# Performance work log

Measured on AMD Instinct MI355X. Metric: run time of the kernel, lower is better.

## Reference

```python
import jax, jax.numpy as jnp
import numpy as np

EPS = 1e-5  # torch InstanceNorm2d default eps

def instance_norm(x):
    # per-sample, per-channel normalization over spatial dims (affine=False)
    m = jnp.mean(x, axis=(2, 3), keepdims=True)
    v = jnp.var(x, axis=(2, 3), keepdims=True)
    return (x - m) * jax.lax.rsqrt(v + EPS)

def conv2d(x, w, b, stride, pad):
    y = jax.lax.conv_general_dilated(
        x, w, (stride, stride), [(pad, pad), (pad, pad)],
        dimension_numbers=('NCHW', 'OIHW', 'NCHW'))
    return y + b[None, :, None, None]

def res_block(x, w1, b1, w2, b2):
    out = conv2d(jax.nn.relu(instance_norm(x)), w1, b1, 1, 1)
    out = conv2d(jax.nn.relu(instance_norm(out)), w2, b2, 1, 1)
    return out + x

def res_block_strided(x, w1, b1, w2, b2, ws, bs):
    out = conv2d(jax.nn.relu(instance_norm(x)), w1, b1, 2, 1)
    out = conv2d(jax.nn.relu(instance_norm(out)), w2, b2, 1, 1)
    return out + conv2d(x, ws, bs, 2, 0)  # 1x1 strided skip projection

def setup_inputs() -> dict:
    key = jax.random.key(0)
    ks = jax.random.split(key, 12)
    B, N, C, H, W = 64, 1, 3, 256, 256
    TEXT, EMB, F, HEADS = 256, 512, 32, 5
    FH, FW = H // 16, W // 16  # 16, 16
    def rn(k, shape, scale=0.05):
        return jax.random.normal(k, shape, dtype=jnp.float32) * scale
    z = lambda *s: jnp.zeros(s, jnp.float32)
    return {
        'x': jax.random.normal(ks[0], (B, N, C, H, W), jnp.float32),
        'text_vector': jax.random.normal(ks[1], (B, TEXT), jnp.float32),
        'conv1_w': rn(ks[2], (F, C, 7, 7)),
        'conv1_b': z(F),
        'rbs_w1': rn(ks[3], (3, F, F, 3, 3)),  # 3 strided resblocks
        'rbs_b1': z(3, F),
        'rbs_w2': rn(ks[4], (3, F, F, 3, 3)),
        'rbs_b2': z(3, F),
        'rbs_ws': rn(ks[5], (3, F, F, 1, 1)),
        'rbs_bs': z(3, F),
        'rb_w1': rn(ks[6], (2, F, F, 3, 3)),  # 2 plain resblocks
        'rb_b1': z(2, F),
        'rb_w2': rn(ks[7], (2, F, F, 3, 3)),
        'rb_b2': z(2, F),
        'attn_w': rn(ks[8], (HEADS, FH * FW, TEXT)),  # torch Linear [out,in] per head
        'attn_b': z(HEADS, FH * FW),
        'final_w': rn(ks[9], (EMB, FH * FW * HEADS)),
        'final_b': z(EMB),
    }

def reference(x, text_vector, conv1_w, conv1_b, rbs_w1, rbs_b1, rbs_w2, rbs_b2,
              rbs_ws, rbs_bs, rb_w1, rb_b1, rb_w2, rb_b2, attn_w, attn_b,
              final_w, final_b):
    B, N, C, H, W = x.shape
    feat = x.reshape(B, N * C, H, W)
    feat = instance_norm(feat)
    feat = conv2d(feat, conv1_w, conv1_b, 2, 3)
    # block1 = strided + plain; block2 = strided + plain; block3 = strided
    feat = res_block_strided(feat, rbs_w1[0], rbs_b1[0], rbs_w2[0], rbs_b2[0], rbs_ws[0], rbs_bs[0])
    feat = res_block(feat, rb_w1[0], rb_b1[0], rb_w2[0], rb_b2[0])
    feat = res_block_strided(feat, rbs_w1[1], rbs_b1[1], rbs_w2[1], rbs_b2[1], rbs_ws[1], rbs_bs[1])
    feat = res_block(feat, rb_w1[1], rb_b1[1], rb_w2[1], rb_b2[1])
    feat = res_block_strided(feat, rbs_w1[2], rbs_b1[2], rbs_w2[2], rbs_b2[2], rbs_ws[2], rbs_bs[2])
    # feat: [B, 32, FH, FW]
    HEADS = attn_w.shape[0]
    FH, FW = feat.shape[2], feat.shape[3]
    # sigmoid-gated spatial attention logits per head: [B, HEADS, FH, FW]
    a = jax.nn.sigmoid(jnp.einsum('bt,hot->bho', text_vector, attn_w) + attn_b[None])
    a = a.reshape(B, HEADS, FH, FW)
    # channel scores: spatial sum of gate * feature -> [B, HEADS, C]
    scores = jnp.einsum('bhij,bcij->bhc', a, feat)
    probs = jax.nn.softmax(scores, axis=-1)  # old F.softmax over channel dim
    # weighted channel sum -> per-head attention map [B, HEADS, FH, FW]
    amaps = jnp.einsum('bhc,bcij->bhij', probs, feat)
    out = amaps.reshape(B, -1) @ final_w.T + final_b
    return out
```

## Files before the change

### kernel.cpp

```cpp
#include <hip/hip_runtime.h>
#include <cstdint>
#include <cstddef>

#define INORM_EPS 1e-5f

typedef _Float16 f16;
typedef f16 f16x8 __attribute__((ext_vector_type(8)));
typedef f16 f16x4 __attribute__((ext_vector_type(4)));
typedef float f32x4 __attribute__((ext_vector_type(4)));

__global__ __launch_bounds__(256) void prep_stats(
    const float* __restrict__ rbs_w1, const float* __restrict__ rbs_w2,
    const float* __restrict__ rb_w1, const float* __restrict__ rb_w2,
    const float* __restrict__ rbs_ws, const float* __restrict__ conv1_w,
    const float* __restrict__ x, float2* __restrict__ SP,
    f16* __restrict__ wp3, f16* __restrict__ wp1, f16* __restrict__ wp7,
    float2* __restrict__ SPx8) {
  const int bx = blockIdx.x;
  if (bx >= 480) {
    const int g = bx - 480;
    const int map = g >> 3, chunk = g & 7;
    const float4* p = (const float4*)(x + (size_t)map * 65536 + (size_t)chunk * 8192);
    float s = 0.f, ss = 0.f;
    for (int i = threadIdx.x; i < 2048; i += 256) {
      float4 v = p[i];
      s += v.x + v.y + v.z + v.w;
      ss += v.x * v.x + v.y * v.y + v.z * v.z + v.w * v.w;
    }
    __shared__ float r0[256], r1[256];
    r0[threadIdx.x] = s;
    r1[threadIdx.x] = ss;
    __syncthreads();
    for (int off = 128; off > 0; off >>= 1) {
      if ((int)threadIdx.x < off) {
        r0[threadIdx.x] += r0[threadIdx.x + off];
        r1[threadIdx.x] += r1[threadIdx.x + off];
      }
      __syncthreads();
    }
    if (threadIdx.x == 0) SPx8[map * 8 + chunk] = make_float2(r0[0], r1[0]);
    return;
  }
  int i = bx * 256 + threadIdx.x;
  if (i < 20480) { SP[i] = make_float2(0.f, 0.f); return; }
  i -= 20480;
  if (i < 92160) {
    int mat = i / 9216, r = i % 9216;
    int p = r >> 10, f = (r >> 9) & 1, l = (r >> 3) & 63, j = r & 7;
    int co = f * 16 + (l & 15), ci = (l >> 4) * 8 + j;
    const float* src; int m;
    if (mat < 3) { src = rbs_w1; m = mat; }
    else if (mat < 6) { src = rbs_w2; m = mat - 3; }
    else if (mat < 8) { src = rb_w1; m = mat - 6; }
    else { src = rb_w2; m = mat - 8; }
    wp3[i] = (f16)src[m * 9216 + co * 288 + ci * 9 + p];
    return;
  }
  i -= 92160;
  if (i < 3072) {
    int mat = i / 1024, r = i % 1024;
    int f = r >> 9, l = (r >> 3) & 63, j = r & 7;
    wp1[i] = (f16)rbs_ws[mat * 1024 + (f * 16 + (l & 15)) * 32 + (l >> 4) * 8 + j];
    return;
  }
  i -= 3072;
  if (i >= 7168) return;
  int ky = i >> 10, f = (i >> 9) & 1, l = (i >> 3) & 63, j = i & 7;
  int k = (l >> 4) * 8 + j, kx = k >> 2, ci = k & 3;
  float v = 0.f;
  if (kx < 7 && ci < 3) v = conv1_w[(f * 16 + (l & 15)) * 147 + ci * 49 + ky * 7 + kx];
  wp7[i] = (f16)v;
}

template <int W, int SKIP, int RPB>
__global__ __launch_bounds__(256) void conv3r(
    const f16* __restrict__ Rin, const float2* __restrict__ SPin, float inv_hw,
    const f16* __restrict__ wp, const float* __restrict__ bias,
    const float* __restrict__ bias2, const f16* __restrict__ skip,
    const f16* __restrict__ wps, f16* __restrict__ Rout,
    float2* __restrict__ ostats) {
  constexpr int TPR = W / 16;
  constexpr int LEN = (RPB * TPR) / 4;
  const int t = threadIdx.x, w = t >> 6, l = t & 63;
  const int n = l & 15, q = l >> 4;
  const int b = blockIdx.z;
  const int tx = w % TPR;
  const int y0 = blockIdx.x * RPB + (w / TPR) * LEN;
  const int x = (tx << 4) + n;
  const f16* Rb = Rin + (size_t)b * W * W * 32;

  f16x8 sc, sh;
#pragma unroll
  for (int j = 0; j < 8; j++) {
    float2 s = SPin[b * 32 + q * 8 + j];
    float mean = s.x * inv_hw;
    float rstd = rsqrtf(s.y * inv_hw - mean * mean + INORM_EPS);
    sc[j] = (f16)rstd;
    sh[j] = (f16)(-mean * rstd);
  }

  f16x8 wf[18];
#pragma unroll
  for (int i = 0; i < 18; i++) wf[i] = *(const f16x8*)(wp + i * 512 + l * 8);
  f16x8 wsf0, wsf1;
  if (SKIP == 2) {
    wsf0 = *(const f16x8*)(wps + l * 8);
    wsf1 = *(const f16x8*)(wps + 512 + l * 8);
  }
  float b0 = bias[n], b1 = bias[16 + n];
  if (SKIP == 2) { b0 += bias2[n]; b1 += bias2[16 + n]; }

  f16* ro = Rout + (size_t)b * W * W * 32;
  const f16* sb = skip ? skip + (size_t)b * (SKIP == 2 ? 4 : 1) * W * W * 32 : nullptr;

  bool okc[3];
#pragma unroll
  for (int kx = 0; kx < 3; kx++) okc[kx] = (unsigned)(x + kx - 1) < (unsigned)W;

  auto rowload = [&](int gy, f16x8* dst) {
    int gyc = min(max(gy, 0), W - 1);
#pragma unroll
    for (int kx = 0; kx < 3; kx++) {
      int gxc = min(max(x + kx - 1, 0), W - 1);
      dst[kx] = *(const f16x8*)(Rb + ((size_t)gyc * W + gxc) * 32 + q * 8);
    }
  };
  auto rownorm = [&](int gy, const f16x8* src, f16x8* dst) {
    bool okr = (unsigned)gy < (unsigned)W;
#pragma unroll
    for (int kx = 0; kx < 3; kx++) {
      f16x8 v = src[kx] * sc + sh;
#pragma unroll
      for (int e = 0; e < 8; e++) v[e] = v[e] > (f16)0 ? v[e] : (f16)0;
      f16x8 z = {};
      dst[kx] = (okr && okc[kx]) ? v : z;
    }
  };

  float sm0 = 0.f, sq0 = 0.f, sm1 = 0.f, sq1 = 0.f;
  f16x8 win[9];
  f16x8 pf[3][3];
#pragma unroll
  for (int jj = 0; jj < 3; jj++) rowload(y0 + jj - 1, &win[jj * 3]);
  if (LEN > 1) rowload(y0 + 2, pf[0]);
  if (LEN > 2) rowload(y0 + 3, pf[1]);
#pragma unroll
  for (int jj = 0; jj < 3; jj++) rownorm(y0 + jj - 1, &win[jj * 3], &win[jj * 3]);

#pragma unroll
  for (int i = 0; i < LEN; i++) {
    int y = y0 + i;
    if (i + 3 < LEN) rowload(y0 + i + 4, pf[(i + 2) % 3]);
    f32x4 acc0 = {0.f, 0.f, 0.f, 0.f}, acc1 = {0.f, 0.f, 0.f, 0.f};
#pragma unroll
    for (int ky = 0; ky < 3; ky++) {
      int slot = (i + ky) % 3;
#pragma unroll
      for (int kx = 0; kx < 3; kx++) {
        f16x8 a = win[slot * 3 + kx];
        acc0 = __builtin_amdgcn_mfma_f32_16x16x32_f16(a, wf[2 * (ky * 3 + kx)], acc0, 0, 0, 0);
        acc1 = __builtin_amdgcn_mfma_f32_16x16x32_f16(a, wf[2 * (ky * 3 + kx) + 1], acc1, 0, 0, 0);
      }
    }
    if (SKIP == 2) {
      const int Ws = 2 * W;
      f16x8 as = *(const f16x8*)(sb + ((size_t)(2 * y) * Ws + 2 * x) * 32 + q * 8);
      acc0 = __builtin_amdgcn_mfma_f32_16x16x32_f16(as, wsf0, acc0, 0, 0, 0);
      acc1 = __builtin_amdgcn_mfma_f32_16x16x32_f16(as, wsf1, acc1, 0, 0, 0);
    }
#pragma unroll
    for (int r = 0; r < 4; r++) {
      size_t px = (size_t)y * W + (tx << 4) + q * 4 + r;
      float v0 = acc0[r] + b0;
      float v1 = acc1[r] + b1;
      if (SKIP == 1) {
        v0 += (float)sb[px * 32 + n];
        v1 += (float)sb[px * 32 + 16 + n];
      }
      ro[px * 32 + n] = (f16)v0;
      ro[px * 32 + 16 + n] = (f16)v1;
      sm0 += v0; sq0 += v0 * v0;
      sm1 += v1; sq1 += v1 * v1;
    }
    if (i + 1 < LEN) rownorm(y0 + i + 2, pf[i % 3], &win[(i % 3) * 3]);
  }
  if (ostats) {
    sm0 += __shfl_xor(sm0, 16); sm0 += __shfl_xor(sm0, 32);
    sq0 += __shfl_xor(sq0, 16); sq0 += __shfl_xor(sq0, 32);
    sm1 += __shfl_xor(sm1, 16); sm1 += __shfl_xor(sm1, 32);
    sq1 += __shfl_xor(sq1, 16); sq1 += __shfl_xor(sq1, 32);
    if (l < 16) {
      atomicAdd(&ostats[b * 32 + n].x, sm0);
      atomicAdd(&ostats[b * 32 + n].y, sq0);
      atomicAdd(&ostats[b * 32 + 16 + n].x, sm1);
      atomicAdd(&ostats[b * 32 + 16 + n].y, sq1);
    }
  }
}

template <int WIN, int STRIDE, int SKIP, int RPB>
__global__ __launch_bounds__(256) void conv3n(
    const f16* __restrict__ Rin, const float2* __restrict__ SPin, float inv_hw,
    const f16* __restrict__ wp, const float* __restrict__ bias,
    const float* __restrict__ bias2, const f16* __restrict__ skip,
    const f16* __restrict__ wps, f16* __restrict__ Rout,
    float2* __restrict__ ostats) {
  constexpr int WOUT = WIN / STRIDE;
  constexpr int TPR = WOUT / 16;
  constexpr int UNITS = TPR * RPB;
  constexpr int U = UNITS / 4;
  static_assert(U >= 1, "need at least one unit per wave");
  constexpr int NB = (U >= 3) ? 3 : ((U >= 2) ? 2 : 1);
  const int t = threadIdx.x, w = t >> 6, l = t & 63;
  const int n = l & 15, q = l >> 4;
  const int b = blockIdx.z;
  const int yb = blockIdx.x * RPB;
  const f16* Rb = Rin + (size_t)b * WIN * WIN * 32;

  f16x8 sc, sh;
#pragma unroll
  for (int j = 0; j < 8; j++) {
    float2 s = SPin[b * 32 + q * 8 + j];
    float mean = s.x * inv_hw;
    float rstd = rsqrtf(s.y * inv_hw - mean * mean + INORM_EPS);
    sc[j] = (f16)rstd;
    sh[j] = (f16)(-mean * rstd);
  }

  f16x8 wf[18];
#pragma unroll
  for (int i = 0; i < 18; i++) wf[i] = *(const f16x8*)(wp + i * 512 + l * 8);
  f16x8 wsf0, wsf1;
  if (SKIP == 2) {
    wsf0 = *(const f16x8*)(wps + l * 8);
    wsf1 = *(const f16x8*)(wps + 512 + l * 8);
  }
  float b0 = bias[n], b1 = bias[16 + n];
  if (SKIP == 2) { b0 += bias2[n]; b1 += bias2[16 + n]; }

  f16* ro = Rout + (size_t)b * WOUT * WOUT * 32;
  const f16* sb = skip ? skip + (size_t)b * (SKIP == 2 ? 4 : 1) * WOUT * WOUT * 32 : nullptr;

  auto load_u = [&](int u, f16x8* a) {
    int ty = u / TPR, tx = u % TPR;
    int y = yb + ty;
#pragma unroll
    for (int kx = 0; kx < 3; kx++) {
      int gx = STRIDE * ((tx << 4) + n) + kx - 1;
      int gxc = min(max(gx, 0), WIN - 1);
#pragma unroll
      for (int ky = 0; ky < 3; ky++) {
        int gy = STRIDE * y + ky - 1;
        int gyc = min(max(gy, 0), WIN - 1);
        a[ky * 3 + kx] = *(const f16x8*)(Rb + ((size_t)gyc * WIN + gxc) * 32 + q * 8);
      }
    }
  };
  auto norm_u = [&](int u, f16x8* a) {
    int ty = u / TPR, tx = u % TPR;
    int y = yb + ty;
#pragma unroll
    for (int kx = 0; kx < 3; kx++) {
      int gx = STRIDE * ((tx << 4) + n) + kx - 1;
      bool okx = (unsigned)gx < (unsigned)WIN;
#pragma unroll
      for (int ky = 0; ky < 3; ky++) {
        int gy = STRIDE * y + ky - 1;
        bool ok = okx && ((unsigned)gy < (unsigned)WIN);
        f16x8 v = a[ky * 3 + kx] * sc + sh;
#pragma unroll
        for (int e = 0; e < 8; e++) v[e] = v[e] > (f16)0 ? v[e] : (f16)0;
        f16x8 z = {};
        a[ky * 3 + kx] = ok ? v : z;
      }
    }
  };

  float sm0 = 0.f, sq0 = 0.f, sm1 = 0.f, sq1 = 0.f;
  f16x8 buf[NB][9];
  load_u(w, buf[0]);
  if (U > 1) load_u(w + 4, buf[1 % NB]);
#pragma unroll
  for (int i = 0; i < U; i++) {
    int u = w + 4 * i;
    if (i + 2 < U) load_u(u + 8, buf[(i + 2) % NB]);
    f16x8* a = buf[i % NB];
    norm_u(u, a);
    int ty = u / TPR, tx = u % TPR;
    int y = yb + ty, x0 = tx << 4;
    f32x4 acc0 = {0.f, 0.f, 0.f, 0.f}, acc1 = {0.f, 0.f, 0.f, 0.f};
#pragma unroll
    for (int p = 0; p < 9; p++) {
      acc0 = __builtin_amdgcn_mfma_f32_16x16x32_f16(a[p], wf[2 * p], acc0, 0, 0, 0);
      acc1 = __builtin_amdgcn_mfma_f32_16x16x32_f16(a[p], wf[2 * p + 1], acc1, 0, 0, 0);
    }
    if (SKIP == 2) {
      const int Ws = 2 * WOUT;
      f16x8 as = *(const f16x8*)(sb + ((size_t)(2 * y) * Ws + 2 * (x0 + n)) * 32 + q * 8);
      acc0 = __builtin_amdgcn_mfma_f32_16x16x32_f16(as, wsf0, acc0, 0, 0, 0);
      acc1 = __builtin_amdgcn_mfma_f32_16x16x32_f16(as, wsf1, acc1, 0, 0, 0);
    }
#pragma unroll
    for (int r = 0; r < 4; r++) {
      size_t px = (size_t)y * WOUT + x0 + q * 4 + r;
      float v0 = acc0[r] + b0;
      float v1 = acc1[r] + b1;
      if (SKIP == 1) {
        v0 += (float)sb[px * 32 + n];
        v1 += (float)sb[px * 32 + 16 + n];
      }
      ro[px * 32 + n] = (f16)v0;
      ro[px * 32 + 16 + n] = (f16)v1;
      sm0 += v0; sq0 += v0 * v0;
      sm1 += v1; sq1 += v1 * v1;
    }
  }
  if (ostats) {
    sm0 += __shfl_xor(sm0, 16); sm0 += __shfl_xor(sm0, 32);
    sq0 += __shfl_xor(sq0, 16); sq0 += __shfl_xor(sq0, 32);
    sm1 += __shfl_xor(sm1, 16); sm1 += __shfl_xor(sm1, 32);
    sq1 += __shfl_xor(sq1, 16); sq1 += __shfl_xor(sq1, 32);
    if (l < 16) {
      atomicAdd(&ostats[b * 32 + n].x, sm0);
      atomicAdd(&ostats[b * 32 + n].y, sq0);
      atomicAdd(&ostats[b * 32 + 16 + n].x, sm1);
      atomicAdd(&ostats[b * 32 + 16 + n].y, sq1);
    }
  }
}

__global__ __launch_bounds__(256) void conv7(
    const float* __restrict__ x, const float2* __restrict__ SPx8,
    const f16* __restrict__ wp, const float* __restrict__ bias,
    f16* __restrict__ Rout, float2* __restrict__ ostats) {
  __shared__ f16 lds[21 * 131 * 8];
  const int t = threadIdx.x, w = t >> 6, l = t & 63;
  const int n = l & 15, q = l >> 4;
  const int b = blockIdx.z;
  const int yb = blockIdx.x * 8;
  const float* Xb = x + (size_t)b * 3 * 65536;
  float mn[3], rs[3];
#pragma unroll
  for (int ci = 0; ci < 3; ci++) {
    float sx = 0.f, sxx = 0.f;
#pragma unroll
    for (int c = 0; c < 8; c++) {
      float2 v = SPx8[(b * 3 + ci) * 8 + c];
      sx += v.x; sxx += v.y;
    }
    mn[ci] = sx * (1.f / 65536.f);
    rs[ci] = rsqrtf(sxx * (1.f / 65536.f) - mn[ci] * mn[ci] + INORM_EPS);
  }
  f16x8 wf[14];
#pragma unroll
  for (int i = 0; i < 14; i++) wf[i] = *(const f16x8*)(wp + i * 512 + l * 8);
  float b0 = bias[n], b1 = bias[16 + n];

  for (int idx = t; idx < 9 * 262; idx += 256) {
    int ri = idx / 262, cl = idx - ri * 262;
    int row = 2 * yb - 3 + ri, col = cl - 3;
    bool ok = ((unsigned)row < 256u) && ((unsigned)col < 256u);
    f16x4 v = {};
    if (ok) {
      const float* p = Xb + (size_t)row * 256 + col;
      v[0] = (f16)((p[0] - mn[0]) * rs[0]);
      v[1] = (f16)((p[65536] - mn[1]) * rs[1]);
      v[2] = (f16)((p[131072] - mn[2]) * rs[2]);
    }
    *(f16x4*)(lds + ((ri * 131 + (cl >> 1)) * 8) + (cl & 1) * 4) = v;
  }
  __syncthreads();

  float sm0 = 0.f, sq0 = 0.f, sm1 = 0.f, sq1 = 0.f;
  f16* ro = Rout + (size_t)b * 16384 * 32;

  auto compute_chunk = [&](int i0, int i1) {
#pragma unroll
    for (int seg = 0; seg < 2; seg++) {
      const int tx = w + seg * 4;
      const int x0 = tx * 16;
      const int u = x0 + n + q;
      for (int i = i0; i < i1; i++) {
        int y = yb + i;
        f32x4 acc0 = {0.f, 0.f, 0.f, 0.f}, acc1 = {0.f, 0.f, 0.f, 0.f};
#pragma unroll
        for (int ky = 0; ky < 7; ky++) {
          f16x8 a = *(const f16x8*)(lds + ((2 * i + ky) * 131 + u) * 8);
          acc0 = __builtin_amdgcn_mfma_f32_16x16x32_f16(a, wf[2 * ky], acc0, 0, 0, 0);
          acc1 = __builtin_amdgcn_mfma_f32_16x16x32_f16(a, wf[2 * ky + 1], acc1, 0, 0, 0);
        }
#pragma unroll
        for (int r = 0; r < 4; r++) {
          size_t px = (size_t)y * 128 + x0 + q * 4 + r;
          float v0 = acc0[r] + b0;
          float v1 = acc1[r] + b1;
          ro[px * 32 + n] = (f16)v0;
          ro[px * 32 + 16 + n] = (f16)v1;
          sm0 += v0; sq0 += v0 * v0;
          sm1 += v1; sq1 += v1 * v1;
        }
      }
    }
  };

  float ub0[7], ub1[7], ub2[7];
#pragma unroll
  for (int it = 0; it < 7; it++) {
    int idx = t + it * 256;
    int ri = idx / 262, cl = idx - ri * 262;
    int row = 2 * yb + 6 + ri, col = cl - 3;
    bool ok = (idx < 1572) && (row < 256) && ((unsigned)col < 256u);
    const float* p = Xb + (size_t)(ok ? row : 0) * 256 + (ok ? col : 0);
    ub0[it] = p[0];
    ub1[it] = p[65536];
    ub2[it] = p[131072];
  }

  compute_chunk(0, 2);

#pragma unroll
  for (int it = 0; it < 7; it++) {
    int idx = t + it * 256;
    if (idx < 1572) {
      int ri = idx / 262, cl = idx - ri * 262;
      int row = 2 * yb + 6 + ri, col = cl - 3;
      bool ok = (row < 256) && ((unsigned)col < 256u);
      f16x4 v = {};
      if (ok) {
        v[0] = (f16)((ub0[it] - mn[0]) * rs[0]);
        v[1] = (f16)((ub1[it] - mn[1]) * rs[1]);
        v[2] = (f16)((ub2[it] - mn[2]) * rs[2]);
      }
      *(f16x4*)(lds + (((9 + ri) * 131 + (cl >> 1)) * 8) + (cl & 1) * 4) = v;
    }
  }

  float uc0[7], uc1[7], uc2[7];
#pragma unroll
  for (int it = 0; it < 7; it++) {
    int idx = t + it * 256;
    int ri = idx / 262, cl = idx - ri * 262;
    int row = 2 * yb + 12 + ri, col = cl - 3;
    bool ok = (idx < 1572) && (row < 256) && ((unsigned)col < 256u);
    const float* p = Xb + (size_t)(ok ? row : 0) * 256 + (ok ? col : 0);
    uc0[it] = p[0];
    uc1[it] = p[65536];
    uc2[it] = p[131072];
  }
  __syncthreads();

  compute_chunk(2, 5);

#pragma unroll
  for (int it = 0; it < 7; it++) {
    int idx = t + it * 256;
    if (idx < 1572) {
      int ri = idx / 262, cl = idx - ri * 262;
      int row = 2 * yb + 12 + ri, col = cl - 3;
      bool ok = (row < 256) && ((unsigned)col < 256u);
      f16x4 v = {};
      if (ok) {
        v[0] = (f16)((uc0[it] - mn[0]) * rs[0]);
        v[1] = (f16)((uc1[it] - mn[1]) * rs[1]);
        v[2] = (f16)((uc2[it] - mn[2]) * rs[2]);
      }
      *(f16x4*)(lds + (((15 + ri) * 131 + (cl >> 1)) * 8) + (cl & 1) * 4) = v;
    }
  }
  __syncthreads();

  compute_chunk(5, 8);

  sm0 += __shfl_xor(sm0, 16); sm0 += __shfl_xor(sm0, 32);
  sq0 += __shfl_xor(sq0, 16); sq0 += __shfl_xor(sq0, 32);
  sm1 += __shfl_xor(sm1, 16); sm1 += __shfl_xor(sm1, 32);
  sq1 += __shfl_xor(sq1, 16); sq1 += __shfl_xor(sq1, 32);
  if (l < 16) {
    atomicAdd(&ostats[b * 32 + n].x, sm0);
    atomicAdd(&ostats[b * 32 + n].y, sq0);
    atomicAdd(&ostats[b * 32 + 16 + n].x, sm1);
    atomicAdd(&ostats[b * 32 + 16 + n].y, sq1);
  }
}

__global__ __launch_bounds__(256) void gates_kernel(
    const float* __restrict__ text, const float* __restrict__ attn_w,
    const float* __restrict__ attn_b, float* __restrict__ G) {
  __shared__ float s_text[64 * 257];
  __shared__ float s_w[16 * 256];
  const int t = threadIdx.x, wv = t >> 6, lane = t & 63;
  const int o0 = blockIdx.x * 16;
  for (int d = t; d < 16384; d += 256) {
    int b = d >> 8, k = d & 255;
    s_text[b * 257 + k] = text[d];
  }
  for (int d = t; d < 4096; d += 256) s_w[d] = attn_w[(size_t)o0 * 256 + d];
  __syncthreads();
  float acc[4];
#pragma unroll
  for (int j = 0; j < 4; j++) acc[j] = attn_b[o0 + wv * 4 + j];
  for (int k = 0; k < 256; k++) {
    float tv = s_text[lane * 257 + k];
#pragma unroll
    for (int j = 0; j < 4; j++) acc[j] = fmaf(s_w[(wv * 4 + j) * 256 + k], tv, acc[j]);
  }
#pragma unroll
  for (int j = 0; j < 4; j++) {
    int o = o0 + wv * 4 + j;
    G[o * 64 + lane] = 1.f / (1.f + __expf(-acc[j]));
  }
}

__global__ __launch_bounds__(256) void scores_kernel(
    const f16* __restrict__ feat, const float* __restrict__ G,
    float* __restrict__ amapT) {
  __shared__ float s_feat[256 * 33];
  __shared__ float s_gate[1280];
  __shared__ float s_scores[5 * 32];
  __shared__ float s_probs[5 * 32];
  const int b = blockIdx.x;
  const int t = threadIdx.x;

  for (int i = t; i < 8192; i += 256)
    s_feat[(i >> 5) * 33 + (i & 31)] = (float)feat[(size_t)b * 8192 + i];
  for (int i = t; i < 1280; i += 256) s_gate[i] = G[i * 64 + b];
  __syncthreads();

  if (t < 160) {
    int h = t >> 5, c = t & 31;
    float acc = 0.f;
    for (int ij = 0; ij < 256; ij++) acc += s_gate[h * 256 + ij] * s_feat[ij * 33 + c];
    s_scores[t] = acc;
  }
  __syncthreads();

  if (t < 5) {
    float mx = -1e30f;
    for (int c = 0; c < 32; c++) mx = fmaxf(mx, s_scores[t * 32 + c]);
    float sum = 0.f;
    for (int c = 0; c < 32; c++) {
      float e = __expf(s_scores[t * 32 + c] - mx);
      s_probs[t * 32 + c] = e;
      sum += e;
    }
    float inv = 1.f / sum;
    for (int c = 0; c < 32; c++) s_probs[t * 32 + c] *= inv;
  }
  __syncthreads();

  for (int h = 0; h < 5; h++) {
    float acc = 0.f;
    for (int c = 0; c < 32; c++) acc += s_probs[h * 32 + c] * s_feat[t * 33 + c];
    amapT[(h * 256 + t) * 64 + b] = acc;
  }
}

__global__ __launch_bounds__(256) void final_kernel(
    const float* __restrict__ amapT, const float* __restrict__ final_w,
    const float* __restrict__ final_b, float* __restrict__ out) {
  __shared__ float s_w[4 * 1280];
  __shared__ float s_red[4][4][64];
  const int t = threadIdx.x, wv = t >> 6, lane = t & 63;
  const int e0 = blockIdx.x * 4;
  for (int d = t; d < 5120; d += 256) s_w[d] = final_w[(size_t)e0 * 1280 + d];
  __syncthreads();
  const int k0 = wv * 320;
  float acc[4] = {0.f, 0.f, 0.f, 0.f};
  for (int k = k0; k < k0 + 320; k++) {
    float av = amapT[k * 64 + lane];
#pragma unroll
    for (int e = 0; e < 4; e++) acc[e] = fmaf(s_w[e * 1280 + k], av, acc[e]);
  }
#pragma unroll
  for (int e = 0; e < 4; e++) s_red[wv][e][lane] = acc[e];
  __syncthreads();
  if (wv == 0) {
#pragma unroll
    for (int e = 0; e < 4; e++) {
      float v = s_red[0][e][lane] + s_red[1][e][lane] + s_red[2][e][lane] +
                s_red[3][e][lane] + final_b[e0 + e];
      out[(size_t)lane * 512 + e0 + e] = v;
    }
  }
}

extern "C" void kernel_launch(void* const* d_in, const int* in_sizes, int n_in,
                              void* d_out, int out_size, void* d_ws, size_t ws_size,
                              hipStream_t stream) {
  (void)in_sizes; (void)n_in; (void)out_size; (void)ws_size;
  const float* x       = (const float*)d_in[0];
  const float* text    = (const float*)d_in[1];
  const float* conv1_w = (const float*)d_in[2];
  const float* conv1_b = (const float*)d_in[3];
  const float* rbs_w1  = (const float*)d_in[4];
  const float* rbs_b1  = (const float*)d_in[5];
  const float* rbs_w2  = (const float*)d_in[6];
  const float* rbs_b2  = (const float*)d_in[7];
  const float* rbs_ws  = (const float*)d_in[8];
  const float* rbs_bs  = (const float*)d_in[9];
  const float* rb_w1   = (const float*)d_in[10];
  const float* rb_b1   = (const float*)d_in[11];
  const float* rb_w2   = (const float*)d_in[12];
  const float* rb_b2   = (const float*)d_in[13];
  const float* attn_w  = (const float*)d_in[14];
  const float* attn_b  = (const float*)d_in[15];
  const float* final_w = (const float*)d_in[16];
  const float* final_b = (const float*)d_in[17];
  float* out = (float*)d_out;

  char* wsb = (char*)d_ws;
  float2* SPx8 = (float2*)(wsb + 0);
  f16*   R128 = (f16*)(wsb + 35145728);
  f16*   R64a = (f16*)(wsb + 102254592);
  f16*   R64b = (f16*)(wsb + 119031808);
  f16*   R64c = (f16*)(wsb + 135809024);
  f16*   R32a = (f16*)(wsb + 152586240);
  f16*   R32b = (f16*)(wsb + 156780544);
  f16*   R32c = (f16*)(wsb + 160974848);
  f16*   R16a = (f16*)(wsb + 165169152);
  f16*   R16b = (f16*)(wsb + 166217728);
  float2* SP  = (float2*)(wsb + 167266304);
  f16*   wp3  = (f16*)(wsb + 167431680);
  f16*   wp1  = (f16*)(wsb + 167616000);
  f16*   wp7  = (f16*)(wsb + 167622144);
  float* G     = (float*)(wsb + 167636480);
  float* amapT = (float*)(wsb + 167964160);
  float2* SP0 = SP + 0 * 2048;
  float2* SP1 = SP + 1 * 2048;
  float2* SP2 = SP + 2 * 2048;
  float2* SP3 = SP + 3 * 2048;
  float2* SP4 = SP + 4 * 2048;
  float2* SP5 = SP + 5 * 2048;
  float2* SP6 = SP + 6 * 2048;
  float2* SP7 = SP + 7 * 2048;
  float2* SP8 = SP + 8 * 2048;
  float2* SP9 = SP + 9 * 2048;

  prep_stats<<<2016, 256, 0, stream>>>(rbs_w1, rbs_w2, rb_w1, rb_w2, rbs_ws,
                                       conv1_w, x, SP, wp3, wp1, wp7, SPx8);

  conv7<<<dim3(16, 1, 64), 256, 0, stream>>>(x, SPx8, wp7, conv1_b, R128, SP0);

  conv3n<128, 2, 0, 4><<<dim3(16, 1, 64), 256, 0, stream>>>(
      R128, SP0, 1.f / 16384.f, wp3, rbs_b1, nullptr, nullptr, nullptr, R64a, SP1);
  conv3r<64, 2, 8><<<dim3(8, 1, 64), 256, 0, stream>>>(
      R64a, SP1, 1.f / 4096.f, wp3 + 3 * 9216, rbs_b2, rbs_bs, R128, wp1, R64b, SP2);

  conv3r<64, 0, 8><<<dim3(8, 1, 64), 256, 0, stream>>>(
      R64b, SP2, 1.f / 4096.f, wp3 + 6 * 9216, rb_b1, nullptr, nullptr, nullptr, R64c, SP3);
  conv3r<64, 1, 8><<<dim3(8, 1, 64), 256, 0, stream>>>(
      R64c, SP3, 1.f / 4096.f, wp3 + 8 * 9216, rb_b2, nullptr, R64b, nullptr, R64a, SP4);

  conv3n<64, 2, 0, 4><<<dim3(8, 1, 64), 256, 0, stream>>>(
      R64a, SP4, 1.f / 4096.f, wp3 + 1 * 9216, rbs_b1 + 32, nullptr, nullptr, nullptr, R32a, SP5);
  conv3r<32, 2, 8><<<dim3(4, 1, 64), 256, 0, stream>>>(
      R32a, SP5, 1.f / 1024.f, wp3 + 4 * 9216, rbs_b2 + 32, rbs_bs + 32, R64a, wp1 + 1024, R32b, SP6);

  conv3r<32, 0, 8><<<dim3(4, 1, 64), 256, 0, stream>>>(
      R32b, SP6, 1.f / 1024.f, wp3 + 7 * 9216, rb_b1 + 32, nullptr, nullptr, nullptr, R32c, SP7);
  conv3r<32, 1, 8><<<dim3(4, 1, 64), 256, 0, stream>>>(
      R32c, SP7, 1.f / 1024.f, wp3 + 9 * 9216, rb_b2 + 32, nullptr, R32b, nullptr, R32a, SP8);

  conv3n<32, 2, 0, 8><<<dim3(2, 1, 64), 256, 0, stream>>>(
      R32a, SP8, 1.f / 1024.f, wp3 + 2 * 9216, rbs_b1 + 64, nullptr, nullptr, nullptr, R16a, SP9);
  conv3n<16, 1, 2, 8><<<dim3(2, 1, 64), 256, 0, stream>>>(
      R16a, SP9, 1.f / 256.f, wp3 + 5 * 9216, rbs_b2 + 64, rbs_bs + 64, R32a, wp1 + 2048, R16b, nullptr);

  gates_kernel<<<80, 256, 0, stream>>>(text, attn_w, attn_b, G);
  scores_kernel<<<64, 256, 0, stream>>>(R16b, G, amapT);
  final_kernel<<<128, 256, 0, stream>>>(amapT, final_w, final_b, out);
}
```

Measured before the change: 311.7 us.

## Add register-windowed stride-2 conv kernel and reshape conv7 staging chunks

Adds a conv3s2 kernel for the stride-2 3x3 convolutions. It keeps a rolling three-row register window of normalized, ReLU'd inputs loaded straight from global memory, and uses it in place of conv3n for the first two strided blocks, with half the blocks per image. It also changes the conv7 kernel's staged loading of input rows into LDS: the first stage loads fewer rows and a fourth load/compute stage is added, so more of the global loads overlap with MFMA work. The risks are higher register pressure in the new kernel, fewer blocks in the grid, and a possible mistake in the shifted row offsets for the reworked chunks.

```diff
diff --git a/kernel.cpp b/kernel.cpp
--- a/kernel.cpp
+++ b/kernel.cpp
@@ -183,6 +183,119 @@
       sm1 += v1; sq1 += v1 * v1;
     }
     if (i + 1 < LEN) rownorm(y0 + i + 2, pf[i % 3], &win[(i % 3) * 3]);
+  }
+  if (ostats) {
+    sm0 += __shfl_xor(sm0, 16); sm0 += __shfl_xor(sm0, 32);
+    sq0 += __shfl_xor(sq0, 16); sq0 += __shfl_xor(sq0, 32);
+    sm1 += __shfl_xor(sm1, 16); sm1 += __shfl_xor(sm1, 32);
+    sq1 += __shfl_xor(sq1, 16); sq1 += __shfl_xor(sq1, 32);
+    if (l < 16) {
+      atomicAdd(&ostats[b * 32 + n].x, sm0);
+      atomicAdd(&ostats[b * 32 + n].y, sq0);
+      atomicAdd(&ostats[b * 32 + 16 + n].x, sm1);
+      atomicAdd(&ostats[b * 32 + 16 + n].y, sq1);
+    }
+  }
+}
+
+template <int WIN>
+__global__ __launch_bounds__(256) void conv3s2(
+    const f16* __restrict__ Rin, const float2* __restrict__ SPin, float inv_hw,
+    const f16* __restrict__ wp, const float* __restrict__ bias,
+    f16* __restrict__ Rout, float2* __restrict__ ostats) {
+  constexpr int WOUT = WIN / 2;
+  constexpr int TPR = WOUT / 16;
+  constexpr int RPB = 8;
+  constexpr int LEN = (RPB * TPR) / 4;
+  const int t = threadIdx.x, w = t >> 6, l = t & 63;
+  const int n = l & 15, q = l >> 4;
+  const int b = blockIdx.z;
+  const int tx = w % TPR;
+  const int y0 = blockIdx.x * RPB + (w / TPR) * LEN;
+  const int x = (tx << 4) + n;
+  const f16* Rb = Rin + (size_t)b * WIN * WIN * 32;
+
+  f16x8 sc, sh;
+#pragma unroll
+  for (int j = 0; j < 8; j++) {
+    float2 s = SPin[b * 32 + q * 8 + j];
+    float mean = s.x * inv_hw;
+    float rstd = rsqrtf(s.y * inv_hw - mean * mean + INORM_EPS);
+    sc[j] = (f16)rstd;
+    sh[j] = (f16)(-mean * rstd);
+  }
+
+  f16x8 wf[18];
+#pragma unroll
+  for (int i = 0; i < 18; i++) wf[i] = *(const f16x8*)(wp + i * 512 + l * 8);
+  float b0 = bias[n], b1 = bias[16 + n];
+
+  f16* ro = Rout + (size_t)b * WOUT * WOUT * 32;
+
+  bool okc[3];
+#pragma unroll
+  for (int kx = 0; kx < 3; kx++) okc[kx] = (unsigned)(2 * x + kx - 1) < (unsigned)WIN;
+
+  auto rowload = [&](int gy, f16x8* dst) {
+    int gyc = min(max(gy, 0), WIN - 1);
+#pragma unroll
+    for (int kx = 0; kx < 3; kx++) {
+      int gxc = min(max(2 * x + kx - 1, 0), WIN - 1);
+      dst[kx] = *(const f16x8*)(Rb + ((size_t)gyc * WIN + gxc) * 32 + q * 8);
+    }
+  };
+  auto rownorm = [&](int gy, const f16x8* src, f16x8* dst) {
+    bool okr = (unsigned)gy < (unsigned)WIN;
+#pragma unroll
+    for (int kx = 0; kx < 3; kx++) {
+      f16x8 v = src[kx] * sc + sh;
+#pragma unroll
+      for (int e = 0; e < 8; e++) v[e] = v[e] > (f16)0 ? v[e] : (f16)0;
+      f16x8 z = {};
+      dst[kx] = (okr && okc[kx]) ? v : z;
+    }
+  };
+
+  float sm0 = 0.f, sq0 = 0.f, sm1 = 0.f, sq1 = 0.f;
+  f16x8 win[9], pa[3], pb[3];
+#pragma unroll
+  for (int jj = 0; jj < 3; jj++) {
+    rowload(2 * y0 - 1 + jj, pa);
+    rownorm(2 * y0 - 1 + jj, pa, &win[jj * 3]);
+  }
+
+#pragma unroll
+  for (int i = 0; i < LEN; i++) {
+    int y = y0 + i;
+    if (i + 1 < LEN) {
+      rowload(2 * y + 2, pa);
+      rowload(2 * y + 3, pb);
+    }
+    f32x4 acc0 = {0.f, 0.f, 0.f, 0.f}, acc1 = {0.f, 0.f, 0.f, 0.f};
+#pragma unroll
+    for (int ky = 0; ky < 3; ky++) {
+      int slot = (2 * i + ky) % 3;
+#pragma unroll
+      for (int kx = 0; kx < 3; kx++) {
+        f16x8 a = win[slot * 3 + kx];
+        acc0 = __builtin_amdgcn_mfma_f32_16x16x32_f16(a, wf[2 * (ky * 3 + kx)], acc0, 0, 0, 0);
+        acc1 = __builtin_amdgcn_mfma_f32_16x16x32_f16(a, wf[2 * (ky * 3 + kx) + 1], acc1, 0, 0, 0);
+      }
+    }
+#pragma unroll
+    for (int r = 0; r < 4; r++) {
+      size_t px = (size_t)y * WOUT + (tx << 4) + q * 4 + r;
+      float v0 = acc0[r] + b0;
+      float v1 = acc1[r] + b1;
+      ro[px * 32 + n] = (f16)v0;
+      ro[px * 32 + 16 + n] = (f16)v1;
+      sm0 += v0; sq0 += v0 * v0;
+      sm1 += v1; sq1 += v1 * v1;
+    }
+    if (i + 1 < LEN) {
+      rownorm(2 * y + 2, pa, &win[((2 * i + 3) % 3) * 3]);
+      rownorm(2 * y + 3, pb, &win[((2 * i + 4) % 3) * 3]);
+    }
   }
   if (ostats) {
     sm0 += __shfl_xor(sm0, 16); sm0 += __shfl_xor(sm0, 32);
@@ -356,7 +469,7 @@
   for (int i = 0; i < 14; i++) wf[i] = *(const f16x8*)(wp + i * 512 + l * 8);
   float b0 = bias[n], b1 = bias[16 + n];
 
-  for (int idx = t; idx < 9 * 262; idx += 256) {
+  for (int idx = t; idx < 7 * 262; idx += 256) {
     int ri = idx / 262, cl = idx - ri * 262;
     int row = 2 * yb - 3 + ri, col = cl - 3;
     bool ok = ((unsigned)row < 256u) && ((unsigned)col < 256u);
@@ -408,7 +521,7 @@
   for (int it = 0; it < 7; it++) {
     int idx = t + it * 256;
     int ri = idx / 262, cl = idx - ri * 262;
-    int row = 2 * yb + 6 + ri, col = cl - 3;
+    int row = 2 * yb + 4 + ri, col = cl - 3;
     bool ok = (idx < 1572) && (row < 256) && ((unsigned)col < 256u);
     const float* p = Xb + (size_t)(ok ? row : 0) * 256 + (ok ? col : 0);
     ub0[it] = p[0];
@@ -416,14 +529,14 @@
     ub2[it] = p[131072];
   }
 
-  compute_chunk(0, 2);
+  compute_chunk(0, 1);
 
 #pragma unroll
   for (int it = 0; it < 7; it++) {
     int idx = t + it * 256;
     if (idx < 1572) {
       int ri = idx / 262, cl = idx - ri * 262;
-      int row = 2 * yb + 6 + ri, col = cl - 3;
+      int row = 2 * yb + 4 + ri, col = cl - 3;
       bool ok = (row < 256) && ((unsigned)col < 256u);
       f16x4 v = {};
       if (ok) {
@@ -431,7 +544,7 @@
         v[1] = (f16)((ub1[it] - mn[1]) * rs[1]);
         v[2] = (f16)((ub2[it] - mn[2]) * rs[2]);
       }
-      *(f16x4*)(lds + (((9 + ri) * 131 + (cl >> 1)) * 8) + (cl & 1) * 4) = v;
+      *(f16x4*)(lds + (((7 + ri) * 131 + (cl >> 1)) * 8) + (cl & 1) * 4) = v;
     }
   }
 
@@ -440,7 +553,7 @@
   for (int it = 0; it < 7; it++) {
     int idx = t + it * 256;
     int ri = idx / 262, cl = idx - ri * 262;
-    int row = 2 * yb + 12 + ri, col = cl - 3;
+    int row = 2 * yb + 10 + ri, col = cl - 3;
     bool ok = (idx < 1572) && (row < 256) && ((unsigned)col < 256u);
     const float* p = Xb + (size_t)(ok ? row : 0) * 256 + (ok ? col : 0);
     uc0[it] = p[0];
@@ -449,14 +562,14 @@
   }
   __syncthreads();
 
-  compute_chunk(2, 5);
+  compute_chunk(1, 4);
 
 #pragma unroll
   for (int it = 0; it < 7; it++) {
     int idx = t + it * 256;
     if (idx < 1572) {
       int ri = idx / 262, cl = idx - ri * 262;
-      int row = 2 * yb + 12 + ri, col = cl - 3;
+      int row = 2 * yb + 10 + ri, col = cl - 3;
       bool ok = (row < 256) && ((unsigned)col < 256u);
       f16x4 v = {};
       if (ok) {
@@ -464,12 +577,45 @@
         v[1] = (f16)((uc1[it] - mn[1]) * rs[1]);
         v[2] = (f16)((uc2[it] - mn[2]) * rs[2]);
       }
-      *(f16x4*)(lds + (((15 + ri) * 131 + (cl >> 1)) * 8) + (cl & 1) * 4) = v;
-    }
-  }
-  __syncthreads();
-
-  compute_chunk(5, 8);
+      *(f16x4*)(lds + (((13 + ri) * 131 + (cl >> 1)) * 8) + (cl & 1) * 4) = v;
+    }
+  }
+
+  float ud0[3], ud1[3], ud2[3];
+#pragma unroll
+  for (int it = 0; it < 3; it++) {
+    int idx = t + it * 256;
+    int ri = idx / 262, cl = idx - ri * 262;
+    int row = 2 * yb + 16 + ri, col = cl - 3;
+    bool ok = (idx < 524) && (row < 256) && ((unsigned)col < 256u);
+    const float* p = Xb + (size_t)(ok ? row : 0) * 256 + (ok ? col : 0);
+    ud0[it] = p[0];
+    ud1[it] = p[65536];
+    ud2[it] = p[131072];
+  }
+  __syncthreads();
+
+  compute_chunk(4, 7);
+
+#pragma unroll
+  for (int it = 0; it < 3; it++) {
+    int idx = t + it * 256;
+    if (idx < 524) {
+      int ri = idx / 262, cl = idx - ri * 262;
+      int row = 2 * yb + 16 + ri, col = cl - 3;
+      bool ok = (row < 256) && ((unsigned)col < 256u);
+      f16x4 v = {};
+      if (ok) {
+        v[0] = (f16)((ud0[it] - mn[0]) * rs[0]);
+        v[1] = (f16)((ud1[it] - mn[1]) * rs[1]);
+        v[2] = (f16)((ud2[it] - mn[2]) * rs[2]);
+      }
+      *(f16x4*)(lds + (((19 + ri) * 131 + (cl >> 1)) * 8) + (cl & 1) * 4) = v;
+    }
+  }
+  __syncthreads();
+
+  compute_chunk(7, 8);
 
   sm0 += __shfl_xor(sm0, 16); sm0 += __shfl_xor(sm0, 32);
   sq0 += __shfl_xor(sq0, 16); sq0 += __shfl_xor(sq0, 32);
@@ -641,8 +787,8 @@
 
   conv7<<<dim3(16, 1, 64), 256, 0, stream>>>(x, SPx8, wp7, conv1_b, R128, SP0);
 
-  conv3n<128, 2, 0, 4><<<dim3(16, 1, 64), 256, 0, stream>>>(
-      R128, SP0, 1.f / 16384.f, wp3, rbs_b1, nullptr, nullptr, nullptr, R64a, SP1);
+  conv3s2<128><<<dim3(8, 1, 64), 256, 0, stream>>>(
+      R128, SP0, 1.f / 16384.f, wp3, rbs_b1, R64a, SP1);
   conv3r<64, 2, 8><<<dim3(8, 1, 64), 256, 0, stream>>>(
       R64a, SP1, 1.f / 4096.f, wp3 + 3 * 9216, rbs_b2, rbs_bs, R128, wp1, R64b, SP2);
 
@@ -651,8 +797,8 @@
   conv3r<64, 1, 8><<<dim3(8, 1, 64), 256, 0, stream>>>(
       R64c, SP3, 1.f / 4096.f, wp3 + 8 * 9216, rb_b2, nullptr, R64b, nullptr, R64a, SP4);
 
-  conv3n<64, 2, 0, 4><<<dim3(8, 1, 64), 256, 0, stream>>>(
-      R64a, SP4, 1.f / 4096.f, wp3 + 1 * 9216, rbs_b1 + 32, nullptr, nullptr, nullptr, R32a, SP5);
+  conv3s2<64><<<dim3(4, 1, 64), 256, 0, stream>>>(
+      R64a, SP4, 1.f / 4096.f, wp3 + 1 * 9216, rbs_b1 + 32, R32a, SP5);
   conv3r<32, 2, 8><<<dim3(4, 1, 64), 256, 0, stream>>>(
       R32a, SP5, 1.f / 1024.f, wp3 + 4 * 9216, rbs_b2 + 32, rbs_bs + 32, R64a, wp1 + 1024, R32b, SP6);
 
```

Measured after the change: 300.9 us. 3.5% less time.
